# Kernel optimization log

Measured on AMD Instinct MI355X. Metric: run time of the kernel, lower is better.

Reference implementation:

```python
import jax, jax.numpy as jnp
import numpy as np

K = 121          # kernel_size
C = 3            # channels
PAD = (K - 1) // 2  # 60, replicate padding so output matches input spatial size


def setup_inputs() -> dict:
    key = jax.random.key(0)
    k1, k2 = jax.random.split(key)
    x = jax.random.normal(k1, (8, C, 512, 512), dtype=jnp.float32)
    sigma = jax.random.uniform(k2, (), dtype=jnp.float32)
    return {"x": x, "sigma": sigma}


def _gaussian_kernel(sigma):
    # sigma -> sigma*8 + 16, variance = sigma**2 (as in torch forward)
    s = sigma * 8.0 + 16.0
    variance = s * s
    coord = jnp.arange(K, dtype=jnp.float32) - (K - 1) / 2.0  # centered coords
    diff = -(coord[:, None] ** 2 + coord[None, :] ** 2)       # [K,K], -((x-m)^2+(y-m)^2)
    kern = jnp.exp(diff / (2.0 * variance))
    # the 1/(2*pi*variance) prefactor cancels under normalization
    kern = kern / jnp.sum(kern)
    return kern


def reference(x, sigma):
    kern = _gaussian_kernel(sigma)
    # depthwise weights: [out_ch=C, in_ch/groups=1, K, K]
    w = jnp.broadcast_to(kern[None, None, :, :], (C, 1, K, K))
    # replicate padding (torch 'replicate' == jnp 'edge')
    xp = jnp.pad(x, ((0, 0), (0, 0), (PAD, PAD), (PAD, PAD)), mode="edge")
    out = jax.lax.conv_general_dilated(
        xp, w,
        window_strides=(1, 1),
        padding="VALID",
        dimension_numbers=("NCHW", "OIHW", "NCHW"),
        feature_group_count=C,
    )
    return out
```

## Files before the change

### kernel.cpp

```cpp
#include <hip/hip_runtime.h>


#define HH    512
#define WW    512
#define PLANE (512 * 512)
#define NIMG  24
#define ROWF  672

__device__ __forceinline__ void make_weights(const float* __restrict__ sigma,
                                             float* __restrict__ wlds, int tid) {
    if (tid < 128) {
        const float s = sigma[0] * 8.0f + 16.0f;
        const float inv2v = 1.0f / (2.0f * s * s);
        float g = 0.0f;
        if (tid < 121) {
            const float c = (float)tid - 60.0f;
            g = __expf(-c * c * inv2v);
        }
        wlds[tid] = g;
    }
}

__device__ __forceinline__ int swz_off(int col) {
    const int u = col >> 2;
    return ((u ^ ((u >> 3) & 7)) << 2) + (col & 3);
}

#define V_OCT(CUR, NXT, KO)                                               \
    { *(float4*)&wq[0] = *(const float4*)&wlds[(KO) * 8];                 \
      *(float4*)&wq[4] = *(const float4*)&wlds[(KO) * 8 + 4];             \
      _Pragma("unroll")                                                   \
      for (int ki = 0; ki < 8; ++ki) {                                    \
          int rr = r0 - 52 + (KO) * 8 + ki;                               \
          rr = rr < 0 ? 0 : (rr > HH - 1 ? HH - 1 : rr);                  \
          NXT[ki] = *(const float2*)&src[(size_t)rr * WW];                \
          const float wk = wq[ki];                                        \
          _Pragma("unroll")                                               \
          for (int j = 0; j < 8; ++j) {                                   \
              const int idx = ki + j;                                     \
              const float2 v = (idx < 8) ? CUR[idx] : NXT[idx - 8];       \
              vac[j].x += wk * v.x; vac[j].y += wk * v.y;                 \
          }                                                               \
      }                                                                   \
    }

#define LOADG2(DA, DB, G)                                                 \
    { const int u_  = 2 * (G);                                            \
      const int o1_ = (u_ ^ ((u_ >> 3) & 7)) << 2;                        \
      const int o2_ = o1_ ^ 4;                                            \
      *(float4*)&DA[0] = *(const float4*)(bs + o1_);                      \
      *(float4*)&DA[4] = *(const float4*)(bs + o2_);                      \
      *(float4*)&DB[0] = *(const float4*)(bs + o1_ + 256);                \
      *(float4*)&DB[4] = *(const float4*)(bs + o2_ + 256); }

#define H_OCT2(A0, A1, A2, A3, B0, B1, B2, B3, KO)                        \
    { LOADG2(A3, B3, L + (KO) + 3)                                        \
      *(float4*)&wq[0] = *(const float4*)&wlds[(KO) * 8];                 \
      *(float4*)&wq[4] = *(const float4*)&wlds[(KO) * 8 + 4];             \
      _Pragma("unroll")                                                   \
      for (int ki = 0; ki < 8; ++ki) {                                    \
          const float wk = wq[ki];                                        \
          _Pragma("unroll")                                               \
          for (int j = 0; j < 8; ++j) {                                   \
              const int idx = ki + j;                                     \
              const float vA = (idx < 8) ? A0[idx]                        \
                             : (idx < 16) ? A1[idx - 8] : A2[idx - 16];   \
              const float vB = (idx < 8) ? B0[idx]                        \
                             : (idx < 16) ? B1[idx - 8] : B2[idx - 16];   \
              accA[j] += wk * vA;                                         \
              accB[j] += wk * vB;                                         \
          }                                                               \
      }                                                                   \
    }

__global__ __launch_bounds__(256, 6) void blur_fused(
        const float* __restrict__ x, const float* __restrict__ sigma,
        float* __restrict__ out) {
    __shared__ float sm[8 * ROWF];
    __shared__ float wlds[128];
    const int tid = threadIdx.x;

    const int lid   = blockIdx.x + gridDim.x * blockIdx.y;
    const int tile  = (lid & 7) * 192 + (lid >> 3);
    const int r0    = (tile & 63) * 8;
    const int plane = tile >> 6;

    const int c0 = tid * 2;
    const float* __restrict__ src = x + (size_t)plane * PLANE + c0;

    float2 wa[8], wb[8], vac[8];
    float  wq[8];
    #pragma unroll
    for (int m = 0; m < 8; ++m) {
        int rr = r0 - 60 + m;
        rr = rr < 0 ? 0 : rr;
        wa[m] = *(const float2*)&src[(size_t)rr * WW];
    }
    make_weights(sigma, wlds, tid);
    #pragma unroll
    for (int j = 0; j < 8; ++j) vac[j] = make_float2(0.f, 0.f);
    __syncthreads();

    const int lane = tid & 63;
    float s_sum = wlds[lane] + wlds[lane + 64];
    #pragma unroll
    for (int o = 32; o >= 1; o >>= 1) s_sum += __shfl_xor(s_sum, o);
    const float inv_s2 = 1.0f / (s_sum * s_sum);

    #pragma unroll 1
    for (int ko = 0; ko < 16; ko += 2) {
        V_OCT(wa, wb, ko)
        V_OCT(wb, wa, ko + 1)
    }

    {
        const int off = swz_off(c0 + 60);
        #pragma unroll
        for (int j = 0; j < 8; ++j)
            *(float2*)&sm[j * ROWF + off] = vac[j];
    }
    __syncthreads();

    if (tid < 36) {
        const int p = (tid < 15) ? tid * 4
                    : (tid < 34) ? 572 + (tid - 15) * 4
                                 : 648 + (tid - 34) * 4;
        const int u   = p >> 2;
        const int off = (u ^ ((u >> 3) & 7)) << 2;
        const int soff = (tid < 15) ? swz_off(60) : swz_off(571);
        #pragma unroll
        for (int r8 = 0; r8 < 8; ++r8) {
            const float v = (tid < 34) ? sm[r8 * ROWF + soff] : 0.0f;
            *(float4*)&sm[r8 * ROWF + off] = make_float4(v, v, v, v);
        }
    }
    __syncthreads();

    const int r = tid >> 5;
    const int L = tid & 31;
    const float* __restrict__ bs = sm + r * ROWF;

    float a0[8], a1[8], a2[8], a3[8];
    float b0[8], b1[8], b2[8], b3[8];
    float accA[8], accB[8];
    #pragma unroll
    for (int j = 0; j < 8; ++j) { accA[j] = 0.0f; accB[j] = 0.0f; }

    LOADG2(a0, b0, L)
    LOADG2(a1, b1, L + 1)
    LOADG2(a2, b2, L + 2)

    #pragma unroll 1
    for (int ko = 0; ko < 16; ko += 4) {
        H_OCT2(a0, a1, a2, a3, b0, b1, b2, b3, ko)
        H_OCT2(a1, a2, a3, a0, b1, b2, b3, b0, ko + 1)
        H_OCT2(a2, a3, a0, a1, b2, b3, b0, b1, ko + 2)
        H_OCT2(a3, a0, a1, a2, b3, b0, b1, b2, ko + 3)
    }

    float* __restrict__ dst = out + (size_t)plane * PLANE
                                  + (size_t)(r0 + r) * WW + L * 8;
    const float k2 = inv_s2;
    *(float4*)(dst)       = make_float4(accA[0] * k2, accA[1] * k2,
                                        accA[2] * k2, accA[3] * k2);
    *(float4*)(dst + 4)   = make_float4(accA[4] * k2, accA[5] * k2,
                                        accA[6] * k2, accA[7] * k2);
    *(float4*)(dst + 256) = make_float4(accB[0] * k2, accB[1] * k2,
                                        accB[2] * k2, accB[3] * k2);
    *(float4*)(dst + 260) = make_float4(accB[4] * k2, accB[5] * k2,
                                        accB[6] * k2, accB[7] * k2);
}

extern "C" void kernel_launch(void* const* d_in, const int* in_sizes, int n_in,
                              void* d_out, int out_size, void* d_ws, size_t ws_size,
                              hipStream_t stream) {
    const float* x     = (const float*)d_in[0];
    const float* sigma = (const float*)d_in[1];
    float* out = (float*)d_out;
    blur_fused<<<dim3(HH / 8, NIMG), dim3(256), 0, stream>>>(x, sigma, out);
}
```

Measured before the change: 119.3 us.

## Widen horizontal pass to 16 contiguous outputs per thread, add interior fast path

The horizontal pass now gives each thread 16 contiguous output columns instead of two separate groups of 8. This cuts the number of LDS group loads per output and lets the sliding register window be shared, so the LDS row can shrink to 640 floats with less padding to fill and the last octave skips its prefetch. The vertical pass gets a separate path for interior row tiles that uses pointer increments and drops the per-row clamp. The wider accumulator set may raise register pressure and lower occupancy.

```diff
diff --git a/kernel.cpp b/kernel.cpp
--- a/kernel.cpp
+++ b/kernel.cpp
@@ -5,7 +5,7 @@
 #define WW    512
 #define PLANE (512 * 512)
 #define NIMG  24
-#define ROWF  672
+#define ROWF  640
 
 __device__ __forceinline__ void make_weights(const float* __restrict__ sigma,
                                              float* __restrict__ wlds, int tid) {
@@ -44,31 +44,57 @@
       }                                                                   \
     }
 
-#define LOADG2(DA, DB, G)                                                 \
+#define V_OCT_NC(CUR, NXT, KO)                                            \
+    { *(float4*)&wq[0] = *(const float4*)&wlds[(KO) * 8];                 \
+      *(float4*)&wq[4] = *(const float4*)&wlds[(KO) * 8 + 4];             \
+      _Pragma("unroll")                                                   \
+      for (int ki = 0; ki < 8; ++ki) {                                    \
+          NXT[ki] = *(const float2*)pv; pv += WW;                         \
+          const float wk = wq[ki];                                        \
+          _Pragma("unroll")                                               \
+          for (int j = 0; j < 8; ++j) {                                   \
+              const int idx = ki + j;                                     \
+              const float2 v = (idx < 8) ? CUR[idx] : NXT[idx - 8];       \
+              vac[j].x += wk * v.x; vac[j].y += wk * v.y;                 \
+          }                                                               \
+      }                                                                   \
+    }
+
+#define LOADG(D, G)                                                       \
     { const int u_  = 2 * (G);                                            \
       const int o1_ = (u_ ^ ((u_ >> 3) & 7)) << 2;                        \
-      const int o2_ = o1_ ^ 4;                                            \
-      *(float4*)&DA[0] = *(const float4*)(bs + o1_);                      \
-      *(float4*)&DA[4] = *(const float4*)(bs + o2_);                      \
-      *(float4*)&DB[0] = *(const float4*)(bs + o1_ + 256);                \
-      *(float4*)&DB[4] = *(const float4*)(bs + o2_ + 256); }
-
-#define H_OCT2(A0, A1, A2, A3, B0, B1, B2, B3, KO)                        \
-    { LOADG2(A3, B3, L + (KO) + 3)                                        \
+      *(float4*)&D[0] = *(const float4*)(bs + o1_);                       \
+      *(float4*)&D[4] = *(const float4*)(bs + (o1_ ^ 4)); }
+
+#define H_OCT(A0, A1, A2, A3, KO)                                         \
+    { LOADG(A3, 2 * L + (KO) + 3)                                         \
       *(float4*)&wq[0] = *(const float4*)&wlds[(KO) * 8];                 \
       *(float4*)&wq[4] = *(const float4*)&wlds[(KO) * 8 + 4];             \
       _Pragma("unroll")                                                   \
       for (int ki = 0; ki < 8; ++ki) {                                    \
           const float wk = wq[ki];                                        \
           _Pragma("unroll")                                               \
-          for (int j = 0; j < 8; ++j) {                                   \
-              const int idx = ki + j;                                     \
-              const float vA = (idx < 8) ? A0[idx]                        \
-                             : (idx < 16) ? A1[idx - 8] : A2[idx - 16];   \
-              const float vB = (idx < 8) ? B0[idx]                        \
-                             : (idx < 16) ? B1[idx - 8] : B2[idx - 16];   \
-              accA[j] += wk * vA;                                         \
-              accB[j] += wk * vB;                                         \
+          for (int j = 0; j < 16; ++j) {                                  \
+              const int idx = ki + j;                                     \
+              const float v = (idx < 8) ? A0[idx]                         \
+                            : (idx < 16) ? A1[idx - 8] : A2[idx - 16];    \
+              acc[j] += wk * v;                                           \
+          }                                                               \
+      }                                                                   \
+    }
+
+#define H_OCT_NP(A0, A1, A2, A3, KO)                                      \
+    { *(float4*)&wq[0] = *(const float4*)&wlds[(KO) * 8];                 \
+      *(float4*)&wq[4] = *(const float4*)&wlds[(KO) * 8 + 4];             \
+      _Pragma("unroll")                                                   \
+      for (int ki = 0; ki < 8; ++ki) {                                    \
+          const float wk = wq[ki];                                        \
+          _Pragma("unroll")                                               \
+          for (int j = 0; j < 16; ++j) {                                  \
+              const int idx = ki + j;                                     \
+              const float v = (idx < 8) ? A0[idx]                         \
+                            : (idx < 16) ? A1[idx - 8] : A2[idx - 16];    \
+              acc[j] += wk * v;                                           \
           }                                                               \
       }                                                                   \
     }
@@ -90,11 +116,18 @@
 
     float2 wa[8], wb[8], vac[8];
     float  wq[8];
-    #pragma unroll
-    for (int m = 0; m < 8; ++m) {
-        int rr = r0 - 60 + m;
-        rr = rr < 0 ? 0 : rr;
-        wa[m] = *(const float2*)&src[(size_t)rr * WW];
+    const bool interior = (r0 >= 64) && (r0 <= 432);
+    if (interior) {
+        const float* pp = src + (size_t)(r0 - 60) * WW;
+        #pragma unroll
+        for (int m = 0; m < 8; ++m) { wa[m] = *(const float2*)pp; pp += WW; }
+    } else {
+        #pragma unroll
+        for (int m = 0; m < 8; ++m) {
+            int rr = r0 - 60 + m;
+            rr = rr < 0 ? 0 : rr;
+            wa[m] = *(const float2*)&src[(size_t)rr * WW];
+        }
     }
     make_weights(sigma, wlds, tid);
     #pragma unroll
@@ -107,10 +140,19 @@
     for (int o = 32; o >= 1; o >>= 1) s_sum += __shfl_xor(s_sum, o);
     const float inv_s2 = 1.0f / (s_sum * s_sum);
 
-    #pragma unroll 1
-    for (int ko = 0; ko < 16; ko += 2) {
-        V_OCT(wa, wb, ko)
-        V_OCT(wb, wa, ko + 1)
+    if (interior) {
+        const float* pv = src + (size_t)(r0 - 52) * WW;
+        #pragma unroll 1
+        for (int ko = 0; ko < 16; ko += 2) {
+            V_OCT_NC(wa, wb, ko)
+            V_OCT_NC(wb, wa, ko + 1)
+        }
+    } else {
+        #pragma unroll 1
+        for (int ko = 0; ko < 16; ko += 2) {
+            V_OCT(wa, wb, ko)
+            V_OCT(wb, wa, ko + 1)
+        }
     }
 
     {
@@ -121,16 +163,14 @@
     }
     __syncthreads();
 
-    if (tid < 36) {
-        const int p = (tid < 15) ? tid * 4
-                    : (tid < 34) ? 572 + (tid - 15) * 4
-                                 : 648 + (tid - 34) * 4;
+    if (tid < 32) {
+        const int p = (tid < 15) ? tid * 4 : 572 + (tid - 15) * 4;
         const int u   = p >> 2;
         const int off = (u ^ ((u >> 3) & 7)) << 2;
         const int soff = (tid < 15) ? swz_off(60) : swz_off(571);
         #pragma unroll
         for (int r8 = 0; r8 < 8; ++r8) {
-            const float v = (tid < 34) ? sm[r8 * ROWF + soff] : 0.0f;
+            const float v = sm[r8 * ROWF + soff];
             *(float4*)&sm[r8 * ROWF + off] = make_float4(v, v, v, v);
         }
     }
@@ -141,34 +181,37 @@
     const float* __restrict__ bs = sm + r * ROWF;
 
     float a0[8], a1[8], a2[8], a3[8];
-    float b0[8], b1[8], b2[8], b3[8];
-    float accA[8], accB[8];
+    float acc[16];
     #pragma unroll
-    for (int j = 0; j < 8; ++j) { accA[j] = 0.0f; accB[j] = 0.0f; }
-
-    LOADG2(a0, b0, L)
-    LOADG2(a1, b1, L + 1)
-    LOADG2(a2, b2, L + 2)
+    for (int j = 0; j < 16; ++j) acc[j] = 0.0f;
+
+    LOADG(a0, 2 * L)
+    LOADG(a1, 2 * L + 1)
+    LOADG(a2, 2 * L + 2)
 
     #pragma unroll 1
-    for (int ko = 0; ko < 16; ko += 4) {
-        H_OCT2(a0, a1, a2, a3, b0, b1, b2, b3, ko)
-        H_OCT2(a1, a2, a3, a0, b1, b2, b3, b0, ko + 1)
-        H_OCT2(a2, a3, a0, a1, b2, b3, b0, b1, ko + 2)
-        H_OCT2(a3, a0, a1, a2, b3, b0, b1, b2, ko + 3)
-    }
+    for (int ko = 0; ko < 12; ko += 4) {
+        H_OCT(a0, a1, a2, a3, ko)
+        H_OCT(a1, a2, a3, a0, ko + 1)
+        H_OCT(a2, a3, a0, a1, ko + 2)
+        H_OCT(a3, a0, a1, a2, ko + 3)
+    }
+    H_OCT   (a0, a1, a2, a3, 12)
+    H_OCT   (a1, a2, a3, a0, 13)
+    H_OCT   (a2, a3, a0, a1, 14)
+    H_OCT_NP(a3, a0, a1, a2, 15)
 
     float* __restrict__ dst = out + (size_t)plane * PLANE
-                                  + (size_t)(r0 + r) * WW + L * 8;
+                                  + (size_t)(r0 + r) * WW + L * 16;
     const float k2 = inv_s2;
-    *(float4*)(dst)       = make_float4(accA[0] * k2, accA[1] * k2,
-                                        accA[2] * k2, accA[3] * k2);
-    *(float4*)(dst + 4)   = make_float4(accA[4] * k2, accA[5] * k2,
-                                        accA[6] * k2, accA[7] * k2);
-    *(float4*)(dst + 256) = make_float4(accB[0] * k2, accB[1] * k2,
-                                        accB[2] * k2, accB[3] * k2);
-    *(float4*)(dst + 260) = make_float4(accB[4] * k2, accB[5] * k2,
-                                        accB[6] * k2, accB[7] * k2);
+    *(float4*)(dst)      = make_float4(acc[0]  * k2, acc[1]  * k2,
+                                       acc[2]  * k2, acc[3]  * k2);
+    *(float4*)(dst + 4)  = make_float4(acc[4]  * k2, acc[5]  * k2,
+                                       acc[6]  * k2, acc[7]  * k2);
+    *(float4*)(dst + 8)  = make_float4(acc[8]  * k2, acc[9]  * k2,
+                                       acc[10] * k2, acc[11] * k2);
+    *(float4*)(dst + 12) = make_float4(acc[12] * k2, acc[13] * k2,
+                                       acc[14] * k2, acc[15] * k2);
 }
 
 extern "C" void kernel_launch(void* const* d_in, const int* in_sizes, int n_in,
```

After: 133.4 us. 11.8% more time.
